# Optimization experiments

Measured on AMD Instinct MI355X. Metric: run time of the kernel, lower is better.

## Reference

```python
import jax, jax.numpy as jnp
import numpy as np


def setup_inputs() -> dict:
    key = jax.random.key(0)
    k1, k2 = jax.random.split(key)
    B, N, C, H, W = 64, 8, 256, 4, 4
    pred = jax.random.normal(k1, (B, N, C, H, W), dtype=jnp.float32)
    gt = jax.random.normal(k2, (B, N, C, H, W), dtype=jnp.float32)
    return {"pred": pred, "gt": gt}


def reference(pred, gt):
    B, N, C, H, W = pred.shape
    M = B * N * H * W
    # pred.permute(0,1,3,4,2).reshape(M, C)
    p = jnp.transpose(pred, (0, 1, 3, 4, 2)).reshape(M, C)
    # gt.permute(2,0,1,3,4).reshape(C, M)
    g = jnp.transpose(gt, (2, 0, 1, 3, 4)).reshape(C, M)
    logits = p @ g  # (M, M)
    # CrossEntropyLoss with targets = arange(M): mean of (logsumexep(row) - diag)
    lse = jax.nn.logsumexp(logits, axis=1)
    diag = jnp.diagonal(logits)
    loss = jnp.mean(lse - diag)
    return loss
```

## Files before the change

### kernel.cpp

```cpp
#include <hip/hip_runtime.h>
#include <hip/hip_bf16.h>
#include <stdint.h>

typedef int   i32x4  __attribute__((ext_vector_type(4)));
typedef int   v8i    __attribute__((ext_vector_type(8)));
typedef float f32x4  __attribute__((ext_vector_type(4)));
typedef float f32x16 __attribute__((ext_vector_type(16)));

#define LOG2E   1.4426950408889634f
#define LN2     0.6931471805599453f
#define C_SCALED 86.56170245f
#define SCALE1  0x7F7F7F7F

__device__ __forceinline__ void gload_lds16(const void* gsrc, void* ldst) {
    __builtin_amdgcn_global_load_lds(
        (const __attribute__((address_space(1))) unsigned int*)gsrc,
        (__attribute__((address_space(3))) unsigned int*)ldst,
        16, 0, 0);
}

__global__ void convert_perm(const float* __restrict__ pred, const float* __restrict__ gt,
                             unsigned char* __restrict__ Ab, unsigned char* __restrict__ Bb,
                             unsigned int* __restrict__ counter)
{
    if (blockIdx.x == 0 && threadIdx.x == 0) *counter = 0u;
    const int slab = blockIdx.x & 511;
    const bool isA = blockIdx.x < 512;
    const float scale = isA ? LOG2E : 1.0f;
    const float* src = (isA ? pred : gt) + (size_t)slab * 4096;
    unsigned char* dst = (isA ? Ab : Bb) + (size_t)slab * 4096;
    const int t  = threadIdx.x;
    const int hw = t >> 4;
    const int c0 = (t & 15) * 16;
    int d[4];
    #pragma unroll
    for (int q = 0; q < 4; ++q) {
        const float v0 = src[(c0 + q * 4 + 0) * 16 + hw] * scale;
        const float v1 = src[(c0 + q * 4 + 1) * 16 + hw] * scale;
        const float v2 = src[(c0 + q * 4 + 2) * 16 + hw] * scale;
        const float v3 = src[(c0 + q * 4 + 3) * 16 + hw] * scale;
        int r = __builtin_amdgcn_cvt_pk_fp8_f32(v0, v1, 0, false);
        r     = __builtin_amdgcn_cvt_pk_fp8_f32(v2, v3, r, true);
        d[q] = r;
    }
    *(i32x4*)(dst + hw * 256 + c0) = (i32x4){d[0], d[1], d[2], d[3]};
}

__global__ __launch_bounds__(256) __attribute__((amdgpu_waves_per_eu(2, 2)))
void gemm_lse(const unsigned char* __restrict__ Ab, const unsigned char* __restrict__ Bb,
              float* __restrict__ rowsum_part, float* __restrict__ diagy)
{
    __shared__ __align__(16) char lds[32768];
    const int tid  = threadIdx.x;
    const int lane = tid & 63;
    const int w    = tid >> 6;
    const int l31  = lane & 31;
    const int hi   = lane >> 5;

    const int jc = blockIdx.x & 15;
    const int ib = blockIdx.x >> 4;
    const int i0 = ib << 8;
    const int j0 = jc << 9;

    v8i pfr[2][4];
    {
        const unsigned char* base = Ab + (size_t)(i0 + w * 64 + l31) * 256 + hi * 32;
        #pragma unroll
        for (int f = 0; f < 2; ++f)
            #pragma unroll
            for (int ks = 0; ks < 4; ++ks)
                pfr[f][ks] = *(const v8i*)(base + f * 32 * 256 + ks * 64);
    }

    const unsigned char* Bbase = Bb + (size_t)j0 * 256;
    const int ibase = i0 + w * 64;

#define STG_ALL(NSRC, NBUF) { \
    _Pragma("unroll") \
    for (int it_ = 0; it_ < 4; ++it_) { \
        const int ob_ = it_ * 4096 + tid * 16; \
        const int sb_ = ob_ ^ (((ob_ >> 8) & 15) << 4); \
        gload_lds16((NSRC) + sb_, (NBUF) + ob_); \
    } }

    STG_ALL(Bbase, lds);

    float rs[2] = {0.f, 0.f};

#define READB(G, JF) { \
    const char* rp_ = lds + (js & 1) * 16384 + ((JF) * 32 + l31) * 256; \
    const int sx_ = (((JF) * 32 + l31) & 15) << 4; \
    _Pragma("unroll") \
    for (int ks_ = 0; ks_ < 4; ++ks_) { \
        const int ko_ = ks_ * 64 + hi * 32; \
        const i32x4 lo_ = *(const i32x4*)(rp_ + ((ko_     ) ^ sx_)); \
        const i32x4 h_  = *(const i32x4*)(rp_ + ((ko_ + 16) ^ sx_)); \
        G[ks_] = (v8i){lo_[0], lo_[1], lo_[2], lo_[3], h_[0], h_[1], h_[2], h_[3]}; \
    } }

#define MMJ(G, A0, A1) { \
    __builtin_amdgcn_s_setprio(1); \
    _Pragma("unroll") \
    for (int ks_ = 0; ks_ < 4; ++ks_) { \
        A0 = __builtin_amdgcn_mfma_scale_f32_32x32x64_f8f6f4( \
            G[ks_], pfr[0][ks_], A0, 0, 0, 0, SCALE1, 0, SCALE1); \
        A1 = __builtin_amdgcn_mfma_scale_f32_32x32x64_f8f6f4( \
            G[ks_], pfr[1][ks_], A1, 0, 0, 0, SCALE1, 0, SCALE1); \
    } \
    __builtin_amdgcn_s_setprio(0); }

#define ZA16(X) { _Pragma("unroll") for (int r_ = 0; r_ < 16; ++r_) X[r_] = -C_SCALED; }

#define EPJ(ACC, IFR, JF) { \
    const int jb_  = jbase + (JF) * 32; \
    const int ibf_ = ibase + (IFR) * 32; \
    float e_[16]; \
    _Pragma("unroll") for (int r_ = 0; r_ < 16; ++r_) e_[r_] = __builtin_amdgcn_exp2f(ACC[r_]); \
    float s_ = ((e_[0]+e_[1])+(e_[2]+e_[3])) + ((e_[4]+e_[5])+(e_[6]+e_[7])) \
             + ((e_[8]+e_[9])+(e_[10]+e_[11])) + ((e_[12]+e_[13])+(e_[14]+e_[15])); \
    if (ibf_ == jb_) { \
        _Pragma("unroll") \
        for (int r_ = 0; r_ < 16; ++r_) \
            if (((r_ & 3) + 8 * (r_ >> 2) + 4 * hi) == l31) diagy[ibf_ + l31] = ACC[r_]; \
    } \
    rs[IFR] += s_; }

    for (int js = 0; js < 8; ++js) {
        asm volatile("s_waitcnt vmcnt(0)" ::: "memory");
        __builtin_amdgcn_s_barrier();

        char*                nbuf  = lds + ((js + 1) & 1) * 16384;
        const unsigned char* nsrc  = Bbase + (size_t)(js + 1) * 16384;
        const int            jbase = j0 + js * 64;

        v8i g0[4], g1[4];
        f32x16 a00, a10, a01, a11;

        READB(g0, 0);
        if (js < 7) STG_ALL(nsrc, nbuf);
        READB(g1, 1);

        ZA16(a00); ZA16(a10);
        MMJ(g0, a00, a10);
        EPJ(a00, 0, 0); EPJ(a10, 1, 0);

        ZA16(a01); ZA16(a11);
        MMJ(g1, a01, a11);
        EPJ(a01, 0, 1); EPJ(a11, 1, 1);
    }

#undef STG_ALL
#undef READB
#undef MMJ
#undef ZA16
#undef EPJ

    #pragma unroll
    for (int f = 0; f < 2; ++f) {
        float v = rs[f];
        v += __shfl_xor(v, 32);
        if (lane < 32)
            rowsum_part[(size_t)(i0 + w * 64 + f * 32 + lane) * 16 + jc] = v;
    }
}

__global__ __launch_bounds__(1024) void reduce_partial(const float* __restrict__ rowsum_part,
                                                       const float* __restrict__ diagy,
                                                       float* __restrict__ accum,
                                                       unsigned int* __restrict__ counter,
                                                       float* __restrict__ out)
{
    const int i = blockIdx.x * 1024 + threadIdx.x;
    const f32x4* p = (const f32x4*)(rowsum_part + (size_t)i * 16);
    float s = 0.f;
    #pragma unroll
    for (int k = 0; k < 4; ++k) {
        const f32x4 v = p[k];
        s += (v[0] + v[1]) + (v[2] + v[3]);
    }
    float val = __log2f(s) - diagy[i];
    #pragma unroll
    for (int d = 1; d < 64; d <<= 1) val += __shfl_xor(val, d);
    __shared__ float red[16];
    if ((threadIdx.x & 63) == 0) red[threadIdx.x >> 6] = val;
    __syncthreads();
    if (threadIdx.x == 0) {
        float t = 0.f;
        #pragma unroll
        for (int k = 0; k < 16; ++k) t += red[k];
        accum[blockIdx.x] = t;
        __threadfence();
        const unsigned n = atomicAdd(counter, 1u);
        if (n == 7u) {
            float tt = 0.f;
            const volatile float* av = (const volatile float*)accum;
            #pragma unroll
            for (int k = 0; k < 8; ++k) tt += av[k];
            out[0] = LN2 * tt * (1.0f / 8192.0f);
        }
    }
}

extern "C" void kernel_launch(void* const* d_in, const int* in_sizes, int n_in,
                              void* d_out, int out_size, void* d_ws, size_t ws_size,
                              hipStream_t stream) {
    const float* pred = (const float*)d_in[0];
    const float* gt   = (const float*)d_in[1];
    float* out = (float*)d_out;

    char* ws = (char*)d_ws;
    float*         accum       = (float*)(ws);
    unsigned int*  counter     = (unsigned int*)(ws + 0x100);
    float*         diagy       = (float*)(ws + 0x1000);
    float*         rowsum_part = (float*)(ws + 0x10000);
    unsigned char* Ab          = (unsigned char*)(ws + 0x100000);
    unsigned char* Bb          = (unsigned char*)(ws + 0x300000);

    convert_perm<<<1024, 256, 0, stream>>>(pred, gt, Ab, Bb, counter);
    gemm_lse<<<512, 256, 0, stream>>>(Ab, Bb, rowsum_part, diagy);
    reduce_partial<<<8, 1024, 0, stream>>>(rowsum_part, diagy, accum, counter, out);
}
```

Before: 39.38 us.

## Double stage size to 128 columns and prefetch B fragments during epilogue

Each pipeline stage of the fused GEMM+logsumexp kernel now loads 128 B columns into a 32KB half of a 64KB LDS double buffer, where it previously loaded 64. This halves the loop iterations and the barriers and waitcnts per tile. Within a stage, the next B fragment is read from LDS before the exp2 epilogue of the current MFMA results so the LDS read latency is hidden. The 64KB LDS use may limit how many workgroups fit per CU, which the waves_per_eu(2,2) setting already constrains.

New measurement: 88.74 us. 125% more time.

```diff
diff --git a/kernel.cpp b/kernel.cpp
--- a/kernel.cpp
+++ b/kernel.cpp
@@ -50,7 +50,7 @@
 void gemm_lse(const unsigned char* __restrict__ Ab, const unsigned char* __restrict__ Bb,
               float* __restrict__ rowsum_part, float* __restrict__ diagy)
 {
-    __shared__ __align__(16) char lds[32768];
+    __shared__ __align__(16) char lds[65536];
     const int tid  = threadIdx.x;
     const int lane = tid & 63;
     const int w    = tid >> 6;
@@ -77,7 +77,7 @@
 
 #define STG_ALL(NSRC, NBUF) { \
     _Pragma("unroll") \
-    for (int it_ = 0; it_ < 4; ++it_) { \
+    for (int it_ = 0; it_ < 8; ++it_) { \
         const int ob_ = it_ * 4096 + tid * 16; \
         const int sb_ = ob_ ^ (((ob_ >> 8) & 15) << 4); \
         gload_lds16((NSRC) + sb_, (NBUF) + ob_); \
@@ -88,8 +88,9 @@
     float rs[2] = {0.f, 0.f};
 
 #define READB(G, JF) { \
-    const char* rp_ = lds + (js & 1) * 16384 + ((JF) * 32 + l31) * 256; \
-    const int sx_ = (((JF) * 32 + l31) & 15) << 4; \
+    const int  row_ = (JF) * 32 + l31; \
+    const char* rp_ = bufp + row_ * 256; \
+    const int  sx_  = (row_ & 15) << 4; \
     _Pragma("unroll") \
     for (int ks_ = 0; ks_ < 4; ++ks_) { \
         const int ko_ = ks_ * 64 + hi * 32; \
@@ -111,42 +112,52 @@
 
 #define ZA16(X) { _Pragma("unroll") for (int r_ = 0; r_ < 16; ++r_) X[r_] = -C_SCALED; }
 
-#define EPJ(ACC, IFR, JF) { \
-    const int jb_  = jbase + (JF) * 32; \
+#define EPJ(ACC, IFR, JB) { \
     const int ibf_ = ibase + (IFR) * 32; \
     float e_[16]; \
     _Pragma("unroll") for (int r_ = 0; r_ < 16; ++r_) e_[r_] = __builtin_amdgcn_exp2f(ACC[r_]); \
     float s_ = ((e_[0]+e_[1])+(e_[2]+e_[3])) + ((e_[4]+e_[5])+(e_[6]+e_[7])) \
              + ((e_[8]+e_[9])+(e_[10]+e_[11])) + ((e_[12]+e_[13])+(e_[14]+e_[15])); \
-    if (ibf_ == jb_) { \
+    if (ibf_ == (JB)) { \
         _Pragma("unroll") \
         for (int r_ = 0; r_ < 16; ++r_) \
             if (((r_ & 3) + 8 * (r_ >> 2) + 4 * hi) == l31) diagy[ibf_ + l31] = ACC[r_]; \
     } \
     rs[IFR] += s_; }
 
-    for (int js = 0; js < 8; ++js) {
+    for (int js = 0; js < 4; ++js) {
         asm volatile("s_waitcnt vmcnt(0)" ::: "memory");
         __builtin_amdgcn_s_barrier();
 
-        char*                nbuf  = lds + ((js + 1) & 1) * 16384;
-        const unsigned char* nsrc  = Bbase + (size_t)(js + 1) * 16384;
-        const int            jbase = j0 + js * 64;
+        const char*          bufp  = lds + (js & 1) * 32768;
+        char*                nbuf  = lds + ((js + 1) & 1) * 32768;
+        const unsigned char* nsrc  = Bbase + (size_t)(js + 1) * 32768;
+        const int            jbase = j0 + js * 128;
 
         v8i g0[4], g1[4];
-        f32x16 a00, a10, a01, a11;
+        f32x16 a0, a1;
 
         READB(g0, 0);
-        if (js < 7) STG_ALL(nsrc, nbuf);
+        if (js < 3) STG_ALL(nsrc, nbuf);
         READB(g1, 1);
 
-        ZA16(a00); ZA16(a10);
-        MMJ(g0, a00, a10);
-        EPJ(a00, 0, 0); EPJ(a10, 1, 0);
-
-        ZA16(a01); ZA16(a11);
-        MMJ(g1, a01, a11);
-        EPJ(a01, 0, 1); EPJ(a11, 1, 1);
+        ZA16(a0); ZA16(a1);
+        MMJ(g0, a0, a1);
+        READB(g0, 2);
+        EPJ(a0, 0, jbase); EPJ(a1, 1, jbase);
+
+        ZA16(a0); ZA16(a1);
+        MMJ(g1, a0, a1);
+        READB(g1, 3);
+        EPJ(a0, 0, jbase + 32); EPJ(a1, 1, jbase + 32);
+
+        ZA16(a0); ZA16(a1);
+        MMJ(g0, a0, a1);
+        EPJ(a0, 0, jbase + 64); EPJ(a1, 1, jbase + 64);
+
+        ZA16(a0); ZA16(a1);
+        MMJ(g1, a0, a1);
+        EPJ(a0, 0, jbase + 96); EPJ(a1, 1, jbase + 96);
     }
 
 #undef STG_ALL
```
